# Performance work log

Measured on AMD Instinct MI355X. Metric: run time of the kernel, lower is better.

## Reference

```python
import jax, jax.numpy as jnp
import numpy as np

# Module hyperparameters derived from init_kwargs
G = 100          # grid_size = int(n_samples ** gamma) = int(10000 ** 0.5)
K = 3            # KAN_SPLINE_ORDER
NB = G + K       # num_basis = 103
H = (1.5 - (-0.5)) / G
# grid identical for every input feature (torch expands a 1D grid)
GRID = jnp.arange(-K, G + K + 1, dtype=jnp.float32) * H - 0.5  # (G + 2K + 1,)


def bspline_basis(x):
    """Cox-de Boor recursion. x: (B, F) -> (B, F, NB)."""
    g = GRID
    xe = x[..., None]  # (B, F, 1)
    bases = ((xe >= g[:-1]) & (xe < g[1:])).astype(x.dtype)  # (B, F, G+2K)
    for k in range(1, K + 1):
        left = (xe - g[:-(k + 1)]) / jnp.maximum(g[k:-1] - g[:-(k + 1)], 1e-8)
        right = (g[k + 1:] - xe) / jnp.maximum(g[k + 1:] - g[1:-k], 1e-8)
        bases = left * bases[..., :-1] + right * bases[..., 1:]
    return bases  # (B, F, NB)


def kan_layer(x, bw, sw, wb, ws, residual):
    # base path: SiLU activation then linear
    base_out = jax.nn.silu(x) @ bw.T                      # (B, out)
    # spline path: basis expansion then contraction with spline_weight
    spline_out = jnp.einsum('bin,oin->bo', bspline_basis(x), sw)
    out = wb * base_out + ws * spline_out
    return out + x if residual else out


def setup_inputs() -> dict:
    key = jax.random.key(0)
    ks = jax.random.split(key, 16)
    B, D, W = 2048, 64, 243
    inp = {'x': jax.random.uniform(ks[0], (B, D), dtype=jnp.float32)}
    dims = [(D, W), (W, W), (W, W), (W, W), (W, W), (W, 1)]
    for i, (fi, fo) in enumerate(dims):
        kb, ksw = jax.random.split(jax.random.fold_in(key, i + 1))
        inp[f'bw{i}'] = jax.random.normal(kb, (fo, fi), dtype=jnp.float32) * (1.0 / np.sqrt(fi))
        # torch init: uniform(-0.5/G, 0.5/G)
        inp[f'sw{i}'] = jax.random.uniform(ksw, (fo, fi, NB), dtype=jnp.float32,
                                           minval=-0.5 / G, maxval=0.5 / G)
        inp[f'wb{i}'] = jnp.zeros((1,), dtype=jnp.float32)
        inp[f'ws{i}'] = jnp.ones((1,), dtype=jnp.float32)
    return inp


def reference(x, bw0, sw0, wb0, ws0, bw1, sw1, wb1, ws1, bw2, sw2, wb2, ws2,
              bw3, sw3, wb3, ws3, bw4, sw4, wb4, ws4, bw5, sw5, wb5, ws5):
    layers = [
        (bw0, sw0, wb0, ws0, False),  # 64 -> 243 (in != out: no residual)
        (bw1, sw1, wb1, ws1, True),
        (bw2, sw2, wb2, ws2, True),
        (bw3, sw3, wb3, ws3, True),
        (bw4, sw4, wb4, ws4, True),
        (bw5, sw5, wb5, ws5, False),  # 243 -> 1 (use_residual=False)
    ]
    h = x
    for bw, sw, wb, ws, res in layers:
        h = kan_layer(h, bw, sw, wb, ws, res)
    return h
```

## Files before the change

### kernel.cpp

```cpp
#include <hip/hip_runtime.h>
#include <hip/hip_fp16.h>
#include <math.h>

#define BATCH 2048
#define NBAS 103
#define NPAIR 102
#define OUTR 243
#define OUTP 256

typedef _Float16 half2v __attribute__((ext_vector_type(2)));

__device__ __forceinline__ float dot2(unsigned a, unsigned b, float c) {
#if __has_builtin(__builtin_amdgcn_fdot2)
    return __builtin_amdgcn_fdot2(__builtin_bit_cast(half2v, a),
                                  __builtin_bit_cast(half2v, b), c, false);
#else
    __half2 ha = __builtin_bit_cast(__half2, a), hb = __builtin_bit_cast(__half2, b);
    c = fmaf(__low2float(ha), __low2float(hb), c);
    c = fmaf(__high2float(ha), __high2float(hb), c);
    return c;
#endif
}

__device__ __forceinline__ uint4 make_meta(float x, int i) {
    float u = (x + 0.56f) * 50.0f;
    bool inr = (u >= 0.0f) && (u < 106.0f);
    float fj = floorf(u);
    float t = u - fj;
    int j = (int)fj;
    j = j < -1 ? -1 : (j > 106 ? 106 : j);
    float omt = 1.0f - t;
    float t2 = t * t, t3 = t2 * t;
    float w[4];
    w[0] = omt * omt * omt * (1.0f / 6.0f);
    w[1] = (3.0f * t3 - 6.0f * t2 + 4.0f) * (1.0f / 6.0f);
    w[2] = (-3.0f * t3 + 3.0f * t2 + 3.0f * t + 1.0f) * (1.0f / 6.0f);
    w[3] = t3 * (1.0f / 6.0f);
    int idx = j - 3;
    int idxc = idx < 0 ? 0 : (idx > 99 ? 99 : idx);
    int d = idx - idxc;
    float wc[4];
    #pragma unroll
    for (int m = 0; m < 4; ++m) {
        int s = m - d;
        wc[m] = (inr && s >= 0 && s < 4) ? w[s] : 0.0f;
    }
    __half2 w01 = __floats2half2_rn(wc[0], wc[1]);
    __half2 w23 = __floats2half2_rn(wc[2], wc[3]);
    uint4 m4;
    m4.x = __builtin_bit_cast(unsigned, w01);
    m4.y = __builtin_bit_cast(unsigned, w23);
    m4.z = (unsigned)((i * (NPAIR * 4) + idxc) << 6);
    m4.w = (unsigned)(i * NBAS + idxc);
    return m4;
}

__device__ __forceinline__ void pairgen_body64(
    const float* __restrict__ sw, int IN, unsigned* __restrict__ pairT,
    __half (*tile)[106], int i, int obase)
{
    int nl = threadIdx.x & 63;
    int w = threadIdx.x >> 6;
    #pragma unroll
    for (int k = 0; k < 16; ++k) {
        int r = w * 16 + k;
        int o = obase + r;
        if (o < OUTR) {
            const float* p = sw + ((size_t)o * IN + i) * NBAS;
            tile[r][nl] = __float2half(p[nl]);
            if (nl + 64 < NBAS)
                tile[r][nl + 64] = __float2half(p[nl + 64]);
        } else {
            tile[r][nl] = __ushort_as_half((unsigned short)0);
            if (nl + 64 < 106)
                tile[r][nl + 64] = __ushort_as_half((unsigned short)0);
        }
    }
    __syncthreads();
    int ol = threadIdx.x & 63;
    int rg = threadIdx.x >> 6;
    unsigned* dst = pairT + (size_t)i * (NPAIR * 4 * 64) + (size_t)(obase >> 6) * (NPAIR * 64);
    for (int r = 0; r < NPAIR; r += 4) {
        int rr = r + rg;
        if (rr < NPAIR) {
            unsigned lo = __half_as_ushort(tile[ol][rr]);
            unsigned hi = __half_as_ushort(tile[ol][rr + 1]);
            dst[(size_t)rr * 64 + ol] = lo | (hi << 16);
        }
    }
}

__global__ __launch_bounds__(256) void pairgen_kernel(
    const float* __restrict__ sw, int IN, unsigned* __restrict__ pairT)
{
    __shared__ __half tile[64][106];
    pairgen_body64(sw, IN, pairT, tile, blockIdx.x, blockIdx.y * 64);
}

__global__ __launch_bounds__(256) void pairgen_all_kernel(
    const float* __restrict__ sw0, const float* __restrict__ sw1,
    const float* __restrict__ sw2, const float* __restrict__ sw3,
    const float* __restrict__ sw4,
    unsigned* __restrict__ pT0, unsigned* __restrict__ pT1,
    unsigned* __restrict__ pT2, unsigned* __restrict__ pT3,
    unsigned* __restrict__ pT4,
    const float* __restrict__ xin, uint4* __restrict__ meta)
{
    __shared__ __half tile[64][106];
    int bx = blockIdx.x;
    if (bx < 4144) {
        const float* sw; unsigned* pt; int IN; int idx;
        if (bx < 256) { sw = sw0; pt = pT0; IN = 64; idx = bx; }
        else {
            int t = bx - 256;
            int l = t / 972;
            idx = t - l * 972;
            IN = OUTR;
            if (l == 0)      { sw = sw1; pt = pT1; }
            else if (l == 1) { sw = sw2; pt = pT2; }
            else if (l == 2) { sw = sw3; pt = pT3; }
            else             { sw = sw4; pt = pT4; }
        }
        pairgen_body64(sw, IN, pt, tile, idx >> 2, (idx & 3) * 64);
    } else {
        int e = (bx - 4144) * 256 + threadIdx.x;
        int b = e >> 6, i = e & 63;
        meta[e] = make_meta(xin[(size_t)b * 64 + i], i);
    }
}

template <int IN>
__global__ __launch_bounds__(256) void basis_kernel(
    const float* __restrict__ xin, int xstride, uint4* __restrict__ meta,
    float4* __restrict__ zbuf)
{
    int e = blockIdx.x * 256 + threadIdx.x;
    if (zbuf && e < (BATCH * OUTP) / 4) zbuf[e] = make_float4(0.f, 0.f, 0.f, 0.f);
    if (e >= BATCH * IN) return;
    int b = e / IN, i = e - b * IN;
    meta[e] = make_meta(xin[(size_t)b * xstride + i], i);
}

template <bool ADDRES>
__global__ __launch_bounds__(256) void basis_mid_kernel(
    const float* __restrict__ hprev,
    const float* __restrict__ parts,
    uint4* __restrict__ meta, float* __restrict__ hcomb)
{
    int e = blockIdx.x * 256 + threadIdx.x;
    if (e >= BATCH * OUTR) return;
    int b = e / OUTR, i = e - b * OUTR;
    size_t addr = (size_t)b * OUTP + i;
    const size_t PS = (size_t)BATCH * OUTP;
    float h = ADDRES ? hprev[addr] : 0.0f;
    #pragma unroll
    for (int s = 0; s < 8; ++s) h += parts[s * PS + addr];
    hcomb[addr] = h;
    meta[e] = make_meta(h, i);
}

template <bool ADDRES>
__global__ __launch_bounds__(256) void fused_pg_bm_kernel(
    const float* __restrict__ sw, unsigned* __restrict__ pairT,
    const float* __restrict__ hprev, const float* __restrict__ parts,
    uint4* __restrict__ meta, float* __restrict__ hcomb)
{
    if (blockIdx.y == 0) {
        __shared__ __half tile[64][106];
        if (blockIdx.x < 972)
            pairgen_body64(sw, OUTR, pairT, tile, blockIdx.x >> 2, (blockIdx.x & 3) * 64);
    } else {
        int e = blockIdx.x * 256 + threadIdx.x;
        if (e >= BATCH * OUTR) return;
        int b = e / OUTR, i = e - b * OUTR;
        size_t addr = (size_t)b * OUTP + i;
        const size_t PS = (size_t)BATCH * OUTP;
        float h = ADDRES ? hprev[addr] : 0.0f;
        #pragma unroll
        for (int s = 0; s < 8; ++s) h += parts[s * PS + addr];
        hcomb[addr] = h;
        meta[e] = make_meta(h, i);
    }
}

__global__ __launch_bounds__(256) void fused0_kernel(
    const float* __restrict__ sw0, unsigned* __restrict__ pairT,
    const float* __restrict__ xin, uint4* __restrict__ meta)
{
    if (blockIdx.y == 0) {
        __shared__ __half tile[64][106];
        if (blockIdx.x < 256)
            pairgen_body64(sw0, 64, pairT, tile, blockIdx.x >> 2, (blockIdx.x & 3) * 64);
    } else {
        int e = blockIdx.x * 256 + threadIdx.x;
        int b = e >> 6, i = e & 63;
        meta[e] = make_meta(xin[(size_t)b * 64 + i], i);
    }
}

template <int IN>
__global__ __launch_bounds__(256, 8) void layer_store_kernel(
    const unsigned* __restrict__ pairT, const uint4* __restrict__ meta,
    const float* __restrict__ h_in, int hstride,
    const float* __restrict__ bw,
    const float* __restrict__ wbp, const float* __restrict__ wsp,
    float* __restrict__ part)
{
    const int lane = threadIdx.x & 63;
    const int wave = __builtin_amdgcn_readfirstlane(threadIdx.x >> 6);
    const int b0 = blockIdx.y * 8 + wave * 2;
    const int cx = blockIdx.x;
    const int i0 = (IN * cx) >> 3;
    const int i1 = (IN * (cx + 1)) >> 3;
    const unsigned laneoff = ((unsigned)(lane >> 4) * (NPAIR * 64)) + ((unsigned)(lane & 15) << 2);
    const uint4* mp0 = meta + (size_t)b0 * IN;
    const uint4* mp1 = mp0 + IN;
    float a0[4] = {0.f, 0.f, 0.f, 0.f};
    float a1[4] = {0.f, 0.f, 0.f, 0.f};
    #pragma unroll 2
    for (int i = i0; i < i1; ++i) {
        uint4 m0 = mp0[i];
        uint4 m1 = mp1[i];
        const uint4* pA = (const uint4*)(pairT + m0.z + laneoff);
        const uint4* pB = (const uint4*)(pairT + m1.z + laneoff);
        uint4 ra = pA[0];
        uint4 rb = pA[32];
        uint4 rc = pB[0];
        uint4 rd = pB[32];
        a0[0] = dot2(m0.x, ra.x, a0[0]); a0[1] = dot2(m0.x, ra.y, a0[1]);
        a0[2] = dot2(m0.x, ra.z, a0[2]); a0[3] = dot2(m0.x, ra.w, a0[3]);
        a0[0] = dot2(m0.y, rb.x, a0[0]); a0[1] = dot2(m0.y, rb.y, a0[1]);
        a0[2] = dot2(m0.y, rb.z, a0[2]); a0[3] = dot2(m0.y, rb.w, a0[3]);
        a1[0] = dot2(m1.x, rc.x, a1[0]); a1[1] = dot2(m1.x, rc.y, a1[1]);
        a1[2] = dot2(m1.x, rc.z, a1[2]); a1[3] = dot2(m1.x, rc.w, a1[3]);
        a1[0] = dot2(m1.y, rd.x, a1[0]); a1[1] = dot2(m1.y, rd.y, a1[1]);
        a1[2] = dot2(m1.y, rd.z, a1[2]); a1[3] = dot2(m1.y, rd.w, a1[3]);
    }
    float wsv = wsp[0];
    float wbv = wbp[0];
    float4 v0 = make_float4(wsv * a0[0], wsv * a0[1], wsv * a0[2], wsv * a0[3]);
    float4 v1 = make_float4(wsv * a1[0], wsv * a1[1], wsv * a1[2], wsv * a1[3]);
    if (wbv != 0.0f) {
        float* pv0 = &v0.x; float* pv1 = &v1.x;
        for (int c = 0; c < 4; ++c) {
            int o = lane * 4 + c;
            if (o < OUTR) {
                float bs0 = 0.0f, bs1 = 0.0f;
                for (int i = i0; i < i1; ++i) {
                    float x0 = h_in[(size_t)b0 * hstride + i];
                    float x1 = h_in[(size_t)(b0 + 1) * hstride + i];
                    bs0 = fmaf(x0 / (1.0f + expf(-x0)), bw[o * IN + i], bs0);
                    bs1 = fmaf(x1 / (1.0f + expf(-x1)), bw[o * IN + i], bs1);
                }
                pv0[c] += wbv * bs0;
                pv1[c] += wbv * bs1;
            }
        }
    }
    float* d0 = part + ((size_t)cx * BATCH + b0) * OUTP + lane * 4;
    *(float4*)d0 = v0;
    *(float4*)(d0 + OUTP) = v1;
}

template <int IN, bool RES>
__global__ __launch_bounds__(256, 8) void layer_atomic_kernel(
    const unsigned* __restrict__ pairT, const uint4* __restrict__ meta,
    const float* __restrict__ h_in, int hstride,
    const float* __restrict__ bw,
    const float* __restrict__ wbp, const float* __restrict__ wsp,
    float* __restrict__ out)
{
    const int lane = threadIdx.x & 63;
    const int wave = __builtin_amdgcn_readfirstlane(threadIdx.x >> 6);
    const int b = blockIdx.y * 4 + wave;
    const int cx = blockIdx.x;
    const int i0 = (IN * cx) >> 3;
    const int i1 = (IN * (cx + 1)) >> 3;
    const unsigned laneoff = ((unsigned)(lane >> 4) * (NPAIR * 64)) + ((unsigned)(lane & 15) << 2);
    const uint4* mp = meta + (size_t)b * IN;
    float acc[4] = {0.f, 0.f, 0.f, 0.f};
    #pragma unroll 2
    for (int i = i0; i < i1; ++i) {
        uint4 m = mp[i];
        const uint4* pA = (const uint4*)(pairT + m.z + laneoff);
        uint4 ra = pA[0];
        uint4 rb = pA[32];
        acc[0] = dot2(m.x, ra.x, acc[0]); acc[1] = dot2(m.x, ra.y, acc[1]);
        acc[2] = dot2(m.x, ra.z, acc[2]); acc[3] = dot2(m.x, ra.w, acc[3]);
        acc[0] = dot2(m.y, rb.x, acc[0]); acc[1] = dot2(m.y, rb.y, acc[1]);
        acc[2] = dot2(m.y, rb.z, acc[2]); acc[3] = dot2(m.y, rb.w, acc[3]);
    }
    float wsv = wsp[0];
    float wbv = wbp[0];
    #pragma unroll
    for (int c = 0; c < 4; ++c) {
        int o = lane * 4 + c;
        float v = wsv * acc[c];
        if (RES && cx == 0) v += h_in[(size_t)b * hstride + o];
        if (wbv != 0.0f && o < OUTR) {
            float bs = 0.0f;
            for (int i = i0; i < i1; ++i) {
                float xx = h_in[(size_t)b * hstride + i];
                bs = fmaf(xx / (1.0f + expf(-xx)), bw[o * IN + i], bs);
            }
            v += wbv * bs;
        }
        unsafeAtomicAdd(&out[(size_t)b * OUTP + o], v);
    }
}

__global__ __launch_bounds__(256) void final_fused_kernel(
    const float* __restrict__ sw5,
    const float* __restrict__ hprev,
    const float* __restrict__ parts,
    const float* __restrict__ bw5,
    const float* __restrict__ wbp, const float* __restrict__ wsp,
    float* __restrict__ out)
{
    int wave = threadIdx.x >> 6, lane = threadIdx.x & 63;
    int b = blockIdx.x * 4 + wave;
    const size_t PS = (size_t)BATCH * OUTP;
    float s = 0.0f, bs = 0.0f;
    for (int i = lane; i < OUTR; i += 64) {
        size_t addr = (size_t)b * OUTP + i;
        float h = hprev[addr];
        #pragma unroll
        for (int ss = 0; ss < 8; ++ss) h += parts[ss * PS + addr];
        uint4 m = make_meta(h, i);
        __half2 w01 = __builtin_bit_cast(__half2, m.x);
        __half2 w23 = __builtin_bit_cast(__half2, m.y);
        const float* p = sw5 + m.w;
        s += __low2float(w01) * p[0] + __high2float(w01) * p[1]
           + __low2float(w23) * p[2] + __high2float(w23) * p[3];
        bs = fmaf(h / (1.0f + expf(-h)), bw5[i], bs);
    }
    #pragma unroll
    for (int d = 32; d; d >>= 1) {
        s += __shfl_down(s, d, 64);
        bs += __shfl_down(bs, d, 64);
    }
    if (lane == 0) out[b] = wsp[0] * s + wbp[0] * bs;
}

__global__ __launch_bounds__(256) void final_kernel(
    const float* __restrict__ sw5,
    const uint4* __restrict__ meta,
    const float* __restrict__ h, const float* __restrict__ bw5,
    const float* __restrict__ wbp, const float* __restrict__ wsp,
    float* __restrict__ out)
{
    int wave = threadIdx.x >> 6, lane = threadIdx.x & 63;
    int b = blockIdx.x * 4 + wave;
    float s = 0.0f;
    for (int i = lane; i < OUTR; i += 64) {
        uint4 m = meta[(size_t)b * OUTR + i];
        __half2 w01 = __builtin_bit_cast(__half2, m.x);
        __half2 w23 = __builtin_bit_cast(__half2, m.y);
        const float* p = sw5 + m.w;
        s += __low2float(w01) * p[0] + __high2float(w01) * p[1]
           + __low2float(w23) * p[2] + __high2float(w23) * p[3];
    }
    #pragma unroll
    for (int d = 32; d; d >>= 1) s += __shfl_down(s, d, 64);
    if (lane == 0) {
        float v = wsp[0] * s;
        float wbv = wbp[0];
        if (wbv != 0.0f) {
            float bs = 0.0f;
            for (int i = 0; i < OUTR; ++i) {
                float xx = h[(size_t)b * OUTP + i];
                bs = fmaf(xx / (1.0f + expf(-xx)), bw5[i], bs);
            }
            v += wbv * bs;
        }
        out[b] = v;
    }
}

extern "C" void kernel_launch(void* const* d_in, const int* in_sizes, int n_in,
                              void* d_out, int out_size, void* d_ws, size_t ws_size,
                              hipStream_t stream)
{
    const float* x = (const float*)d_in[0];
    const float *bw[6], *sw[6], *wb[6], *ws[6];
    for (int l = 0; l < 6; ++l) {
        bw[l] = (const float*)d_in[1 + 4 * l];
        sw[l] = (const float*)d_in[2 + 4 * l];
        wb[l] = (const float*)d_in[3 + 4 * l];
        ws[l] = (const float*)d_in[4 + 4 * l];
    }
    char* base = (char*)d_ws;
    unsigned* pairT1 = (unsigned*)(base + 0);
    uint4*    meta   = (uint4*)(base + 25380864);
    float*    outp   = (float*)d_out;
    const int NB243 = (BATCH * OUTR + 255) / 256;

    const size_t NEED_ALL = 137142272;
    const size_t NEED_MID = 54315008;
    const size_t NEED_ATM = 37537792;

    if (ws_size >= NEED_ALL) {
        float*    parts  = (float*)(base + 33343488);
        float*    hcA    = (float*)(base + 50120704);
        float*    hcB    = (float*)(base + 52217856);
        unsigned* pairT0 = (unsigned*)(base + 54315008);
        unsigned* pairT2 = (unsigned*)(base + 60999680);
        unsigned* pairT3 = (unsigned*)(base + 86380544);
        unsigned* pairT4 = (unsigned*)(base + 111761408);
        unsigned* pT[5] = {pairT0, pairT1, pairT2, pairT3, pairT4};

        pairgen_all_kernel<<<4656, 256, 0, stream>>>(
            sw[0], sw[1], sw[2], sw[3], sw[4],
            pairT0, pairT1, pairT2, pairT3, pairT4, x, meta);

        layer_store_kernel<64><<<dim3(8, BATCH / 8), 256, 0, stream>>>(
            pairT0, meta, x, 64, bw[0], wb[0], ws[0], parts);

        float* hin = hcA; float* hout = hcB;
        for (int l = 1; l <= 4; ++l) {
            if (l == 1)
                basis_mid_kernel<false><<<NB243, 256, 0, stream>>>(nullptr, parts, meta, hin);
            else
                basis_mid_kernel<true><<<NB243, 256, 0, stream>>>(hout, parts, meta, hin);
            layer_store_kernel<243><<<dim3(8, BATCH / 8), 256, 0, stream>>>(
                pT[l], meta, hin, OUTP, bw[l], wb[l], ws[l], parts);
            float* tmp = hin; hin = hout; hout = tmp;
        }
        final_fused_kernel<<<BATCH / 4, 256, 0, stream>>>(
            sw[5], hout, parts, bw[5], wb[5], ws[5], outp);
    } else if (ws_size >= NEED_MID) {
        float* parts = (float*)(base + 33343488);
        float* hcA   = (float*)(base + 50120704);
        float* hcB   = (float*)(base + 52217856);

        fused0_kernel<<<dim3(512, 2), 256, 0, stream>>>(sw[0], pairT1, x, meta);
        layer_store_kernel<64><<<dim3(8, BATCH / 8), 256, 0, stream>>>(
            pairT1, meta, x, 64, bw[0], wb[0], ws[0], parts);

        float* hin = hcA; float* hout = hcB;
        for (int l = 1; l <= 4; ++l) {
            if (l == 1)
                fused_pg_bm_kernel<false><<<dim3(1944, 2), 256, 0, stream>>>(
                    sw[l], pairT1, nullptr, parts, meta, hin);
            else
                fused_pg_bm_kernel<true><<<dim3(1944, 2), 256, 0, stream>>>(
                    sw[l], pairT1, hout, parts, meta, hin);
            layer_store_kernel<243><<<dim3(8, BATCH / 8), 256, 0, stream>>>(
                pairT1, meta, hin, OUTP, bw[l], wb[l], ws[l], parts);
            float* tmp = hin; hin = hout; hout = tmp;
        }
        final_fused_kernel<<<BATCH / 4, 256, 0, stream>>>(
            sw[5], hout, parts, bw[5], wb[5], ws[5], outp);
    } else {
        if (ws_size < NEED_ATM) return;
        float* hA = (float*)(base + 33343488);
        float* hB = (float*)(base + 35440640);
        pairgen_kernel<<<dim3(64, 4), 256, 0, stream>>>(sw[0], 64, pairT1);
        basis_kernel<64><<<(BATCH * 64) / 256, 256, 0, stream>>>(x, 64, meta, (float4*)hA);
        layer_atomic_kernel<64, false><<<dim3(8, BATCH / 4), 256, 0, stream>>>(
            pairT1, meta, x, 64, bw[0], wb[0], ws[0], hA);
        float* hin = hA; float* hout = hB;
        for (int l = 1; l <= 4; ++l) {
            pairgen_kernel<<<dim3(OUTR, 4), 256, 0, stream>>>(sw[l], OUTR, pairT1);
            basis_kernel<243><<<NB243, 256, 0, stream>>>(hin, OUTP, meta, (float4*)hout);
            layer_atomic_kernel<243, true><<<dim3(8, BATCH / 4), 256, 0, stream>>>(
                pairT1, meta, hin, OUTP, bw[l], wb[l], ws[l], hout);
            float* tmp = hin; hin = hout; hout = tmp;
        }
        basis_kernel<243><<<NB243, 256, 0, stream>>>(hin, OUTP, meta, nullptr);
        final_kernel<<<BATCH / 4, 256, 0, stream>>>(sw[5], meta, hin, bw[5], wb[5], ws[5], outp);
    }
}
```

Before: 412.9 us.

## Process four batch rows per wave and two inputs per pairgen block

The layer_store kernel now gives each wave four batch rows instead of two, so blocks cover 16 rows. Twice as many pairT and meta loads are in flight per wave, and the grid shrinks by half. Pairgen blocks now convert two input features per block using a doubled shared tile, which halves the block count. The cost is more registers and lower occupancy (launch bounds drop from 8 to 4) and more shared memory per pairgen block.

Result: slower. 436.3 us (+5.7%).

```diff
diff --git a/kernel.cpp b/kernel.cpp
--- a/kernel.cpp
+++ b/kernel.cpp
@@ -90,6 +90,53 @@
     }
 }
 
+__device__ __forceinline__ void pairgen_body2i(
+    const float* __restrict__ sw, int IN, unsigned* __restrict__ pairT,
+    __half (*tile)[106], int i0, int obase, int ni)
+{
+    int nl = threadIdx.x & 63;
+    int w = threadIdx.x >> 6;
+    #pragma unroll
+    for (int k = 0; k < 16; ++k) {
+        int r = w * 16 + k;
+        int o = obase + r;
+        if (o < OUTR) {
+            const float* p = sw + ((size_t)o * IN + i0) * NBAS;
+            tile[r][nl] = __float2half(p[nl]);
+            if (nl + 64 < NBAS)
+                tile[r][nl + 64] = __float2half(p[nl + 64]);
+            if (ni == 2) {
+                tile[64 + r][nl] = __float2half(p[NBAS + nl]);
+                if (nl + 64 < NBAS)
+                    tile[64 + r][nl + 64] = __float2half(p[NBAS + nl + 64]);
+            }
+        } else {
+            tile[r][nl] = __ushort_as_half((unsigned short)0);
+            tile[64 + r][nl] = __ushort_as_half((unsigned short)0);
+            if (nl + 64 < 106) {
+                tile[r][nl + 64] = __ushort_as_half((unsigned short)0);
+                tile[64 + r][nl + 64] = __ushort_as_half((unsigned short)0);
+            }
+        }
+    }
+    __syncthreads();
+    int ol = threadIdx.x & 63;
+    int rg = threadIdx.x >> 6;
+    for (int q = 0; q < ni; ++q) {
+        unsigned* dst = pairT + (size_t)(i0 + q) * (NPAIR * 4 * 64)
+                              + (size_t)(obase >> 6) * (NPAIR * 64);
+        const __half* trow = &tile[q * 64 + ol][0];
+        for (int r = 0; r < NPAIR; r += 4) {
+            int rr = r + rg;
+            if (rr < NPAIR) {
+                unsigned lo = __half_as_ushort(trow[rr]);
+                unsigned hi = __half_as_ushort(trow[rr + 1]);
+                dst[(size_t)rr * 64 + ol] = lo | (hi << 16);
+            }
+        }
+    }
+}
+
 __global__ __launch_bounds__(256) void pairgen_kernel(
     const float* __restrict__ sw, int IN, unsigned* __restrict__ pairT)
 {
@@ -106,24 +153,26 @@
     unsigned* __restrict__ pT4,
     const float* __restrict__ xin, uint4* __restrict__ meta)
 {
-    __shared__ __half tile[64][106];
+    __shared__ __half tile[128][106];
     int bx = blockIdx.x;
-    if (bx < 4144) {
+    if (bx < 2080) {
         const float* sw; unsigned* pt; int IN; int idx;
-        if (bx < 256) { sw = sw0; pt = pT0; IN = 64; idx = bx; }
+        if (bx < 128) { sw = sw0; pt = pT0; IN = 64; idx = bx; }
         else {
-            int t = bx - 256;
-            int l = t / 972;
-            idx = t - l * 972;
+            int t = bx - 128;
+            int l = t / 488;
+            idx = t - l * 488;
             IN = OUTR;
             if (l == 0)      { sw = sw1; pt = pT1; }
             else if (l == 1) { sw = sw2; pt = pT2; }
             else if (l == 2) { sw = sw3; pt = pT3; }
             else             { sw = sw4; pt = pT4; }
         }
-        pairgen_body64(sw, IN, pt, tile, idx >> 2, (idx & 3) * 64);
+        int i0 = (idx >> 2) * 2;
+        int ni = (i0 + 1 < IN) ? 2 : 1;
+        pairgen_body2i(sw, IN, pt, tile, i0, (idx & 3) * 64, ni);
     } else {
-        int e = (bx - 4144) * 256 + threadIdx.x;
+        int e = (bx - 2080) * 256 + threadIdx.x;
         int b = e >> 6, i = e & 63;
         meta[e] = make_meta(xin[(size_t)b * 64 + i], i);
     }
@@ -199,7 +248,7 @@
 }
 
 template <int IN>
-__global__ __launch_bounds__(256, 8) void layer_store_kernel(
+__global__ __launch_bounds__(256, 4) void layer_store_kernel(
     const unsigned* __restrict__ pairT, const uint4* __restrict__ meta,
     const float* __restrict__ h_in, int hstride,
     const float* __restrict__ bw,
@@ -208,58 +257,59 @@
 {
     const int lane = threadIdx.x & 63;
     const int wave = __builtin_amdgcn_readfirstlane(threadIdx.x >> 6);
-    const int b0 = blockIdx.y * 8 + wave * 2;
+    const int b0 = blockIdx.y * 16 + wave * 4;
     const int cx = blockIdx.x;
     const int i0 = (IN * cx) >> 3;
     const int i1 = (IN * (cx + 1)) >> 3;
     const unsigned laneoff = ((unsigned)(lane >> 4) * (NPAIR * 64)) + ((unsigned)(lane & 15) << 2);
-    const uint4* mp0 = meta + (size_t)b0 * IN;
-    const uint4* mp1 = mp0 + IN;
-    float a0[4] = {0.f, 0.f, 0.f, 0.f};
-    float a1[4] = {0.f, 0.f, 0.f, 0.f};
+    const uint4* mp = meta + (size_t)b0 * IN;
+    float a[4][4] = {};
     #pragma unroll 2
     for (int i = i0; i < i1; ++i) {
-        uint4 m0 = mp0[i];
-        uint4 m1 = mp1[i];
-        const uint4* pA = (const uint4*)(pairT + m0.z + laneoff);
-        const uint4* pB = (const uint4*)(pairT + m1.z + laneoff);
-        uint4 ra = pA[0];
-        uint4 rb = pA[32];
-        uint4 rc = pB[0];
-        uint4 rd = pB[32];
-        a0[0] = dot2(m0.x, ra.x, a0[0]); a0[1] = dot2(m0.x, ra.y, a0[1]);
-        a0[2] = dot2(m0.x, ra.z, a0[2]); a0[3] = dot2(m0.x, ra.w, a0[3]);
-        a0[0] = dot2(m0.y, rb.x, a0[0]); a0[1] = dot2(m0.y, rb.y, a0[1]);
-        a0[2] = dot2(m0.y, rb.z, a0[2]); a0[3] = dot2(m0.y, rb.w, a0[3]);
-        a1[0] = dot2(m1.x, rc.x, a1[0]); a1[1] = dot2(m1.x, rc.y, a1[1]);
-        a1[2] = dot2(m1.x, rc.z, a1[2]); a1[3] = dot2(m1.x, rc.w, a1[3]);
-        a1[0] = dot2(m1.y, rd.x, a1[0]); a1[1] = dot2(m1.y, rd.y, a1[1]);
-        a1[2] = dot2(m1.y, rd.z, a1[2]); a1[3] = dot2(m1.y, rd.w, a1[3]);
+        uint4 m[4];
+        #pragma unroll
+        for (int r = 0; r < 4; ++r) m[r] = mp[(size_t)r * IN + i];
+        uint4 lo[4], hi[4];
+        #pragma unroll
+        for (int r = 0; r < 4; ++r) {
+            const uint4* p = (const uint4*)(pairT + m[r].z + laneoff);
+            lo[r] = p[0];
+            hi[r] = p[32];
+        }
+        #pragma unroll
+        for (int r = 0; r < 4; ++r) {
+            a[r][0] = dot2(m[r].x, lo[r].x, a[r][0]);
+            a[r][1] = dot2(m[r].x, lo[r].y, a[r][1]);
+            a[r][2] = dot2(m[r].x, lo[r].z, a[r][2]);
+            a[r][3] = dot2(m[r].x, lo[r].w, a[r][3]);
+            a[r][0] = dot2(m[r].y, hi[r].x, a[r][0]);
+            a[r][1] = dot2(m[r].y, hi[r].y, a[r][1]);
+            a[r][2] = dot2(m[r].y, hi[r].z, a[r][2]);
+            a[r][3] = dot2(m[r].y, hi[r].w, a[r][3]);
+        }
     }
     float wsv = wsp[0];
     float wbv = wbp[0];
-    float4 v0 = make_float4(wsv * a0[0], wsv * a0[1], wsv * a0[2], wsv * a0[3]);
-    float4 v1 = make_float4(wsv * a1[0], wsv * a1[1], wsv * a1[2], wsv * a1[3]);
-    if (wbv != 0.0f) {
-        float* pv0 = &v0.x; float* pv1 = &v1.x;
-        for (int c = 0; c < 4; ++c) {
-            int o = lane * 4 + c;
-            if (o < OUTR) {
-                float bs0 = 0.0f, bs1 = 0.0f;
-                for (int i = i0; i < i1; ++i) {
-                    float x0 = h_in[(size_t)b0 * hstride + i];
-                    float x1 = h_in[(size_t)(b0 + 1) * hstride + i];
-                    bs0 = fmaf(x0 / (1.0f + expf(-x0)), bw[o * IN + i], bs0);
-                    bs1 = fmaf(x1 / (1.0f + expf(-x1)), bw[o * IN + i], bs1);
+    #pragma unroll
+    for (int r = 0; r < 4; ++r) {
+        float4 v = make_float4(wsv * a[r][0], wsv * a[r][1], wsv * a[r][2], wsv * a[r][3]);
+        if (wbv != 0.0f) {
+            float* pv = &v.x;
+            for (int c = 0; c < 4; ++c) {
+                int o = lane * 4 + c;
+                if (o < OUTR) {
+                    float bs = 0.0f;
+                    for (int i = i0; i < i1; ++i) {
+                        float xx = h_in[(size_t)(b0 + r) * hstride + i];
+                        bs = fmaf(xx / (1.0f + expf(-xx)), bw[o * IN + i], bs);
+                    }
+                    pv[c] += wbv * bs;
                 }
-                pv0[c] += wbv * bs0;
-                pv1[c] += wbv * bs1;
             }
         }
-    }
-    float* d0 = part + ((size_t)cx * BATCH + b0) * OUTP + lane * 4;
-    *(float4*)d0 = v0;
-    *(float4*)(d0 + OUTP) = v1;
+        float* d = part + ((size_t)cx * BATCH + b0 + r) * OUTP + lane * 4;
+        *(float4*)d = v;
+    }
 }
 
 template <int IN, bool RES>
@@ -409,11 +459,11 @@
         unsigned* pairT4 = (unsigned*)(base + 111761408);
         unsigned* pT[5] = {pairT0, pairT1, pairT2, pairT3, pairT4};
 
-        pairgen_all_kernel<<<4656, 256, 0, stream>>>(
+        pairgen_all_kernel<<<2592, 256, 0, stream>>>(
             sw[0], sw[1], sw[2], sw[3], sw[4],
             pairT0, pairT1, pairT2, pairT3, pairT4, x, meta);
 
-        layer_store_kernel<64><<<dim3(8, BATCH / 8), 256, 0, stream>>>(
+        layer_store_kernel<64><<<dim3(8, BATCH / 16), 256, 0, stream>>>(
             pairT0, meta, x, 64, bw[0], wb[0], ws[0], parts);
 
         float* hin = hcA; float* hout = hcB;
@@ -422,7 +472,7 @@
                 basis_mid_kernel<false><<<NB243, 256, 0, stream>>>(nullptr, parts, meta, hin);
             else
                 basis_mid_kernel<true><<<NB243, 256, 0, stream>>>(hout, parts, meta, hin);
-            layer_store_kernel<243><<<dim3(8, BATCH / 8), 256, 0, stream>>>(
+            layer_store_kernel<243><<<dim3(8, BATCH / 16), 256, 0, stream>>>(
                 pT[l], meta, hin, OUTP, bw[l], wb[l], ws[l], parts);
             float* tmp = hin; hin = hout; hout = tmp;
         }
@@ -434,7 +484,7 @@
         float* hcB   = (float*)(base + 52217856);
 
         fused0_kernel<<<dim3(512, 2), 256, 0, stream>>>(sw[0], pairT1, x, meta);
-        layer_store_kernel<64><<<dim3(8, BATCH / 8), 256, 0, stream>>>(
+        layer_store_kernel<64><<<dim3(8, BATCH / 16), 256, 0, stream>>>(
             pairT1, meta, x, 64, bw[0], wb[0], ws[0], parts);
 
         float* hin = hcA; float* hout = hcB;
@@ -445,7 +495,7 @@
             else
                 fused_pg_bm_kernel<true><<<dim3(1944, 2), 256, 0, stream>>>(
                     sw[l], pairT1, hout, parts, meta, hin);
-            layer_store_kernel<243><<<dim3(8, BATCH / 8), 256, 0, stream>>>(
+            layer_store_kernel<243><<<dim3(8, BATCH / 16), 256, 0, stream>>>(
                 pairT1, meta, hin, OUTP, bw[l], wb[l], ws[l], parts);
             float* tmp = hin; hin = hout; hout = tmp;
         }
```
